# Kernel optimization log

Hardware: AMD Instinct MI355X
Metric: run time of the kernel (lower is better)

The kernel has to match this reference:

```python
import jax, jax.numpy as jnp
import numpy as np


def _gcn_norm(edge_index, num_nodes, dtype):
    # PyG GCNConv.norm: add self-loops (weight 1), symmetric deg^{-1/2} normalization
    row, col = edge_index[0], edge_index[1]
    loop = jnp.arange(num_nodes, dtype=row.dtype)
    row = jnp.concatenate([row, loop])
    col = jnp.concatenate([col, loop])
    ew = jnp.ones(row.shape[0], dtype=dtype)
    deg = jax.ops.segment_sum(ew, row, num_segments=num_nodes)
    dis = jnp.where(deg > 0, jax.lax.rsqrt(deg), 0.0)
    norm = dis[row] * ew * dis[col]
    return row, col, norm


def _masked_gcn_conv(x, row, col, norm, sigma, W, b, num_nodes):
    # mask_features: edge gather -> diff/sigma -> square -> scatter-add -> exp mask
    h = (x[col] - x[row]) / sigma            # [E, F]
    h = norm[:, None] * h * h                # [E, F]
    mask = jax.ops.segment_sum(h, row, num_segments=num_nodes)        # [N, F]
    deg = jax.ops.segment_sum(jnp.ones_like(norm), row, num_segments=num_nodes)  # degree(source), >=1 due to self-loops
    x = x * jnp.exp(-mask / deg[:, None])
    # GCNConv: linear transform then normalized aggregation source->target
    xw = x @ W                               # [N, O]
    out = jax.ops.segment_sum(norm[:, None] * xw[row], col, num_segments=num_nodes)
    return out + b


def setup_inputs() -> dict:
    key = jax.random.key(0)
    ks = jax.random.split(key, 8)
    N, E, F, H, C = 100000, 1600000, 128, 64, 40
    g = 1.414  # xavier gain used for sigma
    return {
        "x": jax.random.normal(ks[0], (N, F), jnp.float32),
        "edge_index": jax.random.randint(ks[1], (2, E), 0, N, jnp.int64),
        "sigma1": jax.random.uniform(ks[2], (1, F), jnp.float32, -1.0, 1.0) * (g * np.sqrt(6.0 / (1 + F))),
        "W1": jax.random.normal(ks[3], (F, H), jnp.float32) * (1.0 / np.sqrt(F)),
        "b1": jnp.zeros((H,), jnp.float32),
        "sigma2": jax.random.uniform(ks[4], (1, H), jnp.float32, -1.0, 1.0) * (g * np.sqrt(6.0 / (1 + H))),
        "W2": jax.random.normal(ks[5], (H, C), jnp.float32) * (1.0 / np.sqrt(H)),
        "b2": jnp.zeros((C,), jnp.float32),
    }


def reference(x, edge_index, sigma1, W1, b1, sigma2, W2, b2):
    N = x.shape[0]
    row, col, norm = _gcn_norm(edge_index, N, x.dtype)
    x = _masked_gcn_conv(x, row, col, norm, sigma1, W1, b1, N)
    x = jax.nn.relu(x)
    # dropout is identity in eval mode
    x = _masked_gcn_conv(x, row, col, norm, sigma2, W2, b2, N)
    return jax.nn.log_softmax(x, axis=1)
```

## Files before the change

### kernel.cpp

```cpp
#include <hip/hip_runtime.h>
#include <cmath>

constexpr int F1 = 128;
constexpr int H  = 64;
constexpr int NC = 40;
constexpr int NXCD = 8;

constexpr int SCAN_TPB = 256;
constexpr int SCAN_IPT = 8;
constexpr int SCAN_EPB = SCAN_TPB * SCAN_IPT;

__device__ inline unsigned short f2bf(float f) {
    union { float f; unsigned u; } v; v.f = f;
    return (unsigned short)((v.u + 0x7FFFu + ((v.u >> 16) & 1u)) >> 16);
}
__device__ inline float bflo(unsigned p) { union { float f; unsigned u; } v; v.u = p << 16; return v.f; }
__device__ inline float bfhi(unsigned p) { union { float f; unsigned u; } v; v.u = p & 0xFFFF0000u; return v.f; }
__device__ inline void unpack8(uint4 raw, float* d) {
    d[0] = bflo(raw.x); d[1] = bfhi(raw.x); d[2] = bflo(raw.y); d[3] = bfhi(raw.y);
    d[4] = bflo(raw.z); d[5] = bfhi(raw.z); d[6] = bflo(raw.w); d[7] = bfhi(raw.w);
}

__global__ void isg_kernel(const float* __restrict__ s1, float* __restrict__ i1,
                           const float* __restrict__ s2, float* __restrict__ i2) {
    int i = threadIdx.x;
    if (i < F1) i1[i] = 1.0f / s1[i];
    if (i < H)  i2[i] = 1.0f / s2[i];
}

__global__ void count8_prep_kernel(const int* __restrict__ row, const int* __restrict__ col,
                                   int* __restrict__ cntO, int* __restrict__ cntI,
                                   int E, int chunk, int stride, int cntBlocks,
                                   const float* __restrict__ x, const float* __restrict__ isg,
                                   unsigned short* __restrict__ u, size_t n8) {
    int bid = blockIdx.x;
    if (bid < cntBlocks) {
        int p = bid & (NXCD - 1);
        int gid = bid >> 3;
        unsigned lo = (unsigned)(p * chunk);
        for (int e = gid * blockDim.x + threadIdx.x; e < E; e += stride) {
            int r = row[e], c = col[e];
            if ((unsigned)r - lo < (unsigned)chunk) atomicAdd(&cntO[r], 1);
            if ((unsigned)c - lo < (unsigned)chunk) atomicAdd(&cntI[c], 1);
        }
    } else {
        size_t idx = (size_t)(bid - cntBlocks) * blockDim.x + threadIdx.x;
        if (idx >= n8) return;
        size_t base = idx * 8;
        int fk = (int)(base % (size_t)F1);
        float4 a0 = *(const float4*)&x[base];
        float4 a1 = *(const float4*)&x[base + 4];
        float4 s0 = *(const float4*)&isg[fk];
        float4 s1 = *(const float4*)&isg[fk + 4];
        uint4 p4;
        p4.x = (unsigned)f2bf(a0.x * s0.x) | ((unsigned)f2bf(a0.y * s0.y) << 16);
        p4.y = (unsigned)f2bf(a0.z * s0.z) | ((unsigned)f2bf(a0.w * s0.w) << 16);
        p4.z = (unsigned)f2bf(a1.x * s1.x) | ((unsigned)f2bf(a1.y * s1.y) << 16);
        p4.w = (unsigned)f2bf(a1.z * s1.z) | ((unsigned)f2bf(a1.w * s1.w) << 16);
        *(uint4*)&u[base] = p4;
    }
}

__global__ void scan_partial_kernel(const int* __restrict__ cnt, int* __restrict__ bsum, int M) {
    __shared__ int red[SCAN_TPB];
    int t = threadIdx.x;
    int i0 = blockIdx.x * SCAN_EPB + t * SCAN_IPT;
    int s = 0;
#pragma unroll
    for (int k = 0; k < SCAN_IPT; ++k) {
        int i = i0 + k;
        if (i < M) s += cnt[i];
    }
    red[t] = s;
    __syncthreads();
    for (int off = SCAN_TPB / 2; off > 0; off >>= 1) {
        if (t < off) red[t] += red[t + off];
        __syncthreads();
    }
    if (t == 0) bsum[blockIdx.x] = red[0];
}

__global__ void scan_offsets_kernel(int* __restrict__ bsum, int nb,
                                    int* __restrict__ rowptrO, int* __restrict__ rowptrI,
                                    int N, int E) {
    __shared__ int sh[1024];
    int t = threadIdx.x;
    sh[t] = (t < nb) ? bsum[t] : 0;
    __syncthreads();
    for (int off = 1; off < 1024; off <<= 1) {
        int v = (t >= off) ? sh[t - off] : 0;
        __syncthreads();
        sh[t] += v;
        __syncthreads();
    }
    if (t < nb) bsum[t] = (t > 0) ? sh[t - 1] : 0;
    if (t == 0) { rowptrO[N] = E; rowptrI[N] = E; }
}

__global__ void scan_final_kernel(int* __restrict__ cntO, int* __restrict__ cntI,
                                  const int* __restrict__ bsum,
                                  int* __restrict__ rowptrO, int* __restrict__ rowptrI,
                                  float* __restrict__ dis, int N, int E) {
    __shared__ int sh[SCAN_TPB];
    int t = threadIdx.x;
    int M = 2 * N;
    const int* cnt = cntO;
    int i0 = blockIdx.x * SCAN_EPB + t * SCAN_IPT;
    int cv[SCAN_IPT], pre[SCAN_IPT];
    int run = 0;
#pragma unroll
    for (int k = 0; k < SCAN_IPT; ++k) {
        int i = i0 + k;
        cv[k] = (i < M) ? cnt[i] : 0;
        pre[k] = run;
        run += cv[k];
    }
    sh[t] = run;
    __syncthreads();
    for (int off = 1; off < SCAN_TPB; off <<= 1) {
        int v = (t >= off) ? sh[t - off] : 0;
        __syncthreads();
        sh[t] += v;
        __syncthreads();
    }
    int toff = ((t > 0) ? sh[t - 1] : 0) + bsum[blockIdx.x];
#pragma unroll
    for (int k = 0; k < SCAN_IPT; ++k) {
        int i = i0 + k;
        if (i < M) {
            int val = toff + pre[k];
            if (i < N) {
                rowptrO[i] = val;
                cntO[i] = val;
                dis[i] = rsqrtf((float)(cv[k] + 1));
            } else {
                rowptrI[i - N] = val - E;
                cntI[i - N] = val - E;
            }
        }
    }
}

__global__ void build8_kernel(const int* __restrict__ row, const int* __restrict__ col,
                              int* __restrict__ curO, int* __restrict__ curI,
                              int2* __restrict__ adjO2, int2* __restrict__ adjI2,
                              const float* __restrict__ dis,
                              int E, int chunk, int stride) {
    int p = blockIdx.x & (NXCD - 1);
    int gid = blockIdx.x >> 3;
    unsigned lo = (unsigned)(p * chunk);
    for (int e = gid * blockDim.x + threadIdx.x; e < E; e += stride) {
        int r = row[e], c = col[e];
        bool inR = (unsigned)r - lo < (unsigned)chunk;
        bool inC = (unsigned)c - lo < (unsigned)chunk;
        if (inR | inC) {
            float nrm = dis[r] * dis[c];
            int nb = __float_as_int(nrm);
            if (inR) adjO2[atomicAdd(&curO[r], 1)] = make_int2(c, nb);
            if (inC) adjI2[atomicAdd(&curI[c], 1)] = make_int2(r, nb);
        }
    }
}

template<int F, int O, int R>
__global__ void fused_mask_gemm_kernel(const int* __restrict__ rowptr, const int2* __restrict__ adj2,
                                       const float* __restrict__ x,
                                       const unsigned short* __restrict__ u,
                                       const float* __restrict__ W,
                                       unsigned short* __restrict__ Ybf, int N) {
    constexpr int NT = R * 64;
    constexpr int G = F / 8;
    constexpr int NPI = 64 / G;
    __shared__ __align__(16) float Ws[F * O];
    __shared__ __align__(16) float Xs[R][F];
    int tid = threadIdx.x;
    for (int i = tid; i < F * O; i += NT) Ws[i] = W[i];
    int w = tid >> 6, lane = tid & 63;
    int h = lane / G, j = lane % G;
    int r = blockIdx.x * R + w;
    if (r < N) {
        int beg = rowptr[r], end = rowptr[r + 1];
        float inv_deg = 1.0f / (float)(end - beg + 1);
        float ur[8], acc[8];
        unpack8(*(const uint4*)&u[(size_t)r * F + 8 * j], ur);
#pragma unroll
        for (int k = 0; k < 8; ++k) acc[k] = 0.0f;
        for (int t = beg; t < end; t += 2 * NPI) {
            int e0 = t + h, e1 = t + NPI + h;
            int2 a0 = adj2[min(e0, end - 1)];
            int2 a1 = adj2[min(e1, end - 1)];
            float n0 = (e0 < end) ? __int_as_float(a0.y) : 0.0f;
            float n1 = (e1 < end) ? __int_as_float(a1.y) : 0.0f;
            uint4 rw0 = *(const uint4*)&u[(size_t)a0.x * F + 8 * j];
            uint4 rw1 = *(const uint4*)&u[(size_t)a1.x * F + 8 * j];
            float uc[8];
            unpack8(rw0, uc);
#pragma unroll
            for (int q = 0; q < 8; ++q) {
                float d = uc[q] - ur[q];
                acc[q] = fmaf(n0 * d, d, acc[q]);
            }
            unpack8(rw1, uc);
#pragma unroll
            for (int q = 0; q < 8; ++q) {
                float d = uc[q] - ur[q];
                acc[q] = fmaf(n1 * d, d, acc[q]);
            }
        }
#pragma unroll
        for (int off = G; off < 64; off <<= 1) {
#pragma unroll
            for (int k = 0; k < 8; ++k) acc[k] += __shfl_xor(acc[k], off);
        }
        if (h == 0) {
            float4 a0 = *(const float4*)&x[(size_t)r * F + 8 * j];
            float4 a1 = *(const float4*)&x[(size_t)r * F + 8 * j + 4];
            float xm[8] = {a0.x, a0.y, a0.z, a0.w, a1.x, a1.y, a1.z, a1.w};
#pragma unroll
            for (int k = 0; k < 8; ++k) xm[k] *= expf(-acc[k] * inv_deg);
            *(float4*)&Xs[w][8 * j]     = make_float4(xm[0], xm[1], xm[2], xm[3]);
            *(float4*)&Xs[w][8 * j + 4] = make_float4(xm[4], xm[5], xm[6], xm[7]);
        }
    }
    __syncthreads();
    if (r < N && lane < O) {
        float acc = 0.0f;
#pragma unroll
        for (int fq = 0; fq < F / 4; ++fq) {
            float4 xs = *(const float4*)&Xs[w][4 * fq];
            acc = fmaf(xs.x, Ws[(4 * fq + 0) * O + lane], acc);
            acc = fmaf(xs.y, Ws[(4 * fq + 1) * O + lane], acc);
            acc = fmaf(xs.z, Ws[(4 * fq + 2) * O + lane], acc);
            acc = fmaf(xs.w, Ws[(4 * fq + 3) * O + lane], acc);
        }
        float other = __shfl_xor(acc, 1);
        if (!(lane & 1)) {
            *(unsigned*)&Ybf[(size_t)r * O + lane] =
                (unsigned)f2bf(acc) | ((unsigned)f2bf(other) << 16);
        }
    }
}

__global__ void agg_relu_kernel(const int* __restrict__ rowptr, const int2* __restrict__ adj2,
                                const float* __restrict__ dis, const unsigned short* __restrict__ ybf,
                                const float* __restrict__ bias, float* __restrict__ h1,
                                unsigned short* __restrict__ u2, const float* __restrict__ isg2, int N) {
    int c = blockIdx.x * (blockDim.x >> 6) + (threadIdx.x >> 6);
    if (c >= N) return;
    int lane = threadIdx.x & 63;
    int h = lane >> 3, j = lane & 7;
    int beg = rowptr[c], end = rowptr[c + 1];
    float acc[8];
#pragma unroll
    for (int k = 0; k < 8; ++k) acc[k] = 0.0f;
    for (int t = beg; t < end; t += 16) {
        int e0 = t + h, e1 = t + 8 + h;
        int2 a0 = adj2[min(e0, end - 1)];
        int2 a1 = adj2[min(e1, end - 1)];
        float n0 = (e0 < end) ? __int_as_float(a0.y) : 0.0f;
        float n1 = (e1 < end) ? __int_as_float(a1.y) : 0.0f;
        uint4 rw0 = *(const uint4*)&ybf[(size_t)a0.x * H + 8 * j];
        uint4 rw1 = *(const uint4*)&ybf[(size_t)a1.x * H + 8 * j];
        float v[8];
        unpack8(rw0, v);
#pragma unroll
        for (int q = 0; q < 8; ++q) acc[q] = fmaf(n0, v[q], acc[q]);
        unpack8(rw1, v);
#pragma unroll
        for (int q = 0; q < 8; ++q) acc[q] = fmaf(n1, v[q], acc[q]);
    }
#pragma unroll
    for (int off = 8; off < 64; off <<= 1) {
#pragma unroll
        for (int k = 0; k < 8; ++k) acc[k] += __shfl_xor(acc[k], off);
    }
    if (h == 0) {
        float dc = dis[c];
        float sv[8];
        unpack8(*(const uint4*)&ybf[(size_t)c * H + 8 * j], sv);
        float4 b0 = *(const float4*)&bias[8 * j];
        float4 b1v = *(const float4*)&bias[8 * j + 4];
        float bb[8] = {b0.x, b0.y, b0.z, b0.w, b1v.x, b1v.y, b1v.z, b1v.w};
        float4 s0 = *(const float4*)&isg2[8 * j];
        float4 s1 = *(const float4*)&isg2[8 * j + 4];
        float sg[8] = {s0.x, s0.y, s0.z, s0.w, s1.x, s1.y, s1.z, s1.w};
        float hv[8];
        float d2 = dc * dc;
#pragma unroll
        for (int k = 0; k < 8; ++k) hv[k] = fmaxf(fmaf(d2, sv[k], acc[k]) + bb[k], 0.0f);
        *(float4*)&h1[(size_t)c * H + 8 * j]     = make_float4(hv[0], hv[1], hv[2], hv[3]);
        *(float4*)&h1[(size_t)c * H + 8 * j + 4] = make_float4(hv[4], hv[5], hv[6], hv[7]);
        uint4 p;
        p.x = (unsigned)f2bf(hv[0] * sg[0]) | ((unsigned)f2bf(hv[1] * sg[1]) << 16);
        p.y = (unsigned)f2bf(hv[2] * sg[2]) | ((unsigned)f2bf(hv[3] * sg[3]) << 16);
        p.z = (unsigned)f2bf(hv[4] * sg[4]) | ((unsigned)f2bf(hv[5] * sg[5]) << 16);
        p.w = (unsigned)f2bf(hv[6] * sg[6]) | ((unsigned)f2bf(hv[7] * sg[7]) << 16);
        *(uint4*)&u2[(size_t)c * H + 8 * j] = p;
    }
}

__global__ void agg_lsm_kernel(const int* __restrict__ rowptr, const int2* __restrict__ adj2,
                               const float* __restrict__ dis, const unsigned short* __restrict__ ybf,
                               const float* __restrict__ bias, float* __restrict__ out, int N) {
    int c = blockIdx.x * (blockDim.x >> 6) + (threadIdx.x >> 6);
    if (c >= N) return;
    int lane = threadIdx.x & 63;
    int h = lane >> 4, j = lane & 15;
    bool active = j < 10;
    int beg = rowptr[c], end = rowptr[c + 1];
    float a[4] = {0.f, 0.f, 0.f, 0.f};
    for (int t = beg; t < end; t += 8) {
        int e0 = t + h, e1 = t + 4 + h;
        int2 a0 = adj2[min(e0, end - 1)];
        int2 a1 = adj2[min(e1, end - 1)];
        float n0 = (e0 < end) ? __int_as_float(a0.y) : 0.0f;
        float n1 = (e1 < end) ? __int_as_float(a1.y) : 0.0f;
        uint2 rw0 = active ? *(const uint2*)&ybf[(size_t)a0.x * NC + 4 * j] : make_uint2(0u, 0u);
        uint2 rw1 = active ? *(const uint2*)&ybf[(size_t)a1.x * NC + 4 * j] : make_uint2(0u, 0u);
        a[0] = fmaf(n0, bflo(rw0.x), a[0]); a[1] = fmaf(n0, bfhi(rw0.x), a[1]);
        a[2] = fmaf(n0, bflo(rw0.y), a[2]); a[3] = fmaf(n0, bfhi(rw0.y), a[3]);
        a[0] = fmaf(n1, bflo(rw1.x), a[0]); a[1] = fmaf(n1, bfhi(rw1.x), a[1]);
        a[2] = fmaf(n1, bflo(rw1.y), a[2]); a[3] = fmaf(n1, bfhi(rw1.y), a[3]);
    }
#pragma unroll
    for (int off = 16; off < 64; off <<= 1) {
#pragma unroll
        for (int k = 0; k < 4; ++k) a[k] += __shfl_xor(a[k], off);
    }
    bool wr = (h == 0) && active;
    float v[4] = {-INFINITY, -INFINITY, -INFINITY, -INFINITY};
    if (wr) {
        float dc = dis[c];
        uint2 sr = *(const uint2*)&ybf[(size_t)c * NC + 4 * j];
        float sv[4] = {bflo(sr.x), bfhi(sr.x), bflo(sr.y), bfhi(sr.y)};
        float4 bb = *(const float4*)&bias[4 * j];
        float b4[4] = {bb.x, bb.y, bb.z, bb.w};
        float d2 = dc * dc;
#pragma unroll
        for (int k = 0; k < 4; ++k) v[k] = fmaf(d2, sv[k], a[k]) + b4[k];
    }
    float m = fmaxf(fmaxf(v[0], v[1]), fmaxf(v[2], v[3]));
#pragma unroll
    for (int off = 8; off > 0; off >>= 1) m = fmaxf(m, __shfl_xor(m, off));
    float s = wr ? (expf(v[0] - m) + expf(v[1] - m) + expf(v[2] - m) + expf(v[3] - m)) : 0.0f;
#pragma unroll
    for (int off = 8; off > 0; off >>= 1) s += __shfl_xor(s, off);
    float mls = m + logf(s);
    if (wr)
        *(float4*)&out[(size_t)c * NC + 4 * j] = make_float4(v[0] - mls, v[1] - mls, v[2] - mls, v[3] - mls);
}

extern "C" void kernel_launch(void* const* d_in, const int* in_sizes, int n_in,
                              void* d_out, int out_size, void* d_ws, size_t ws_size,
                              hipStream_t stream) {
    const float* x    = (const float*)d_in[0];
    const int*   ei   = (const int*)  d_in[1];
    const float* sig1 = (const float*)d_in[2];
    const float* W1   = (const float*)d_in[3];
    const float* b1   = (const float*)d_in[4];
    const float* sig2 = (const float*)d_in[5];
    const float* W2   = (const float*)d_in[6];
    const float* b2   = (const float*)d_in[7];
    float* out = (float*)d_out;

    const int N = in_sizes[0] / F1;
    const int E = in_sizes[1] / 2;
    const int* row = ei;
    const int* col = ei + E;

    char* w = (char*)d_ws;
    auto alloc = [&](size_t bytes) { void* q = w; w += (bytes + 255) & ~255ull; return q; };
    int*   cntO    = (int*)  alloc((size_t)2 * N * 4);
    int*   cntI    = cntO + N;
    int*   rowptrO = (int*)  alloc((size_t)(N + 1) * 4);
    int*   rowptrI = (int*)  alloc((size_t)(N + 1) * 4);
    int2*  adjO2   = (int2*) alloc((size_t)E * 8);
    int2*  adjI2   = (int2*) alloc((size_t)E * 8);
    float* dis     = (float*)alloc((size_t)N * 4);
    float* isg1    = (float*)alloc(F1 * 4);
    float* isg2    = (float*)alloc(H * 4);
    int*   bsum    = (int*)  alloc(1024 * 4);
    unsigned short* u1   = (unsigned short*)alloc((size_t)N * F1 * 2);
    unsigned short* u2   = (unsigned short*)alloc((size_t)N * H * 2);
    unsigned short* ybf1 = (unsigned short*)alloc((size_t)N * H * 2);
    float* h1      = (float*)alloc((size_t)N * H * 4);
    unsigned short* ybf2 = u1;

    const int B = 256;
    const int chunk = (N + NXCD - 1) / NXCD;
    const int WPP = 1024;
    const int stride8 = WPP * B;
    const int cntBlocks = NXCD * WPP;
    const size_t n8 = (size_t)N * F1 / 8;
    const int prepBlocks = (int)((n8 + B - 1) / B);
    const int M = 2 * N;
    const int nb = (M + SCAN_EPB - 1) / SCAN_EPB;

    hipMemsetAsync(cntO, 0, (size_t)2 * N * 4, stream);
    isg_kernel<<<1, 128, 0, stream>>>(sig1, isg1, sig2, isg2);
    count8_prep_kernel<<<cntBlocks + prepBlocks, B, 0, stream>>>(
        row, col, cntO, cntI, E, chunk, stride8, cntBlocks, x, isg1, u1, n8);
    scan_partial_kernel<<<nb, SCAN_TPB, 0, stream>>>(cntO, bsum, M);
    scan_offsets_kernel<<<1, 1024, 0, stream>>>(bsum, nb, rowptrO, rowptrI, N, E);
    scan_final_kernel<<<nb, SCAN_TPB, 0, stream>>>(cntO, cntI, bsum, rowptrO, rowptrI, dis, N, E);
    build8_kernel<<<cntBlocks, B, 0, stream>>>(row, col, cntO, cntI, adjO2, adjI2, dis, E, chunk, stride8);

    fused_mask_gemm_kernel<F1, H, 8><<<(N + 7) / 8, 512, 0, stream>>>(rowptrO, adjO2, x, u1, W1, ybf1, N);
    agg_relu_kernel<<<(N + 3) / 4, B, 0, stream>>>(rowptrI, adjI2, dis, ybf1, b1, h1, u2, isg2, N);

    fused_mask_gemm_kernel<H, NC, 8><<<(N + 7) / 8, 512, 0, stream>>>(rowptrO, adjO2, h1, u2, W2, ybf2, N);
    agg_lsm_kernel<<<(N + 3) / 4, B, 0, stream>>>(rowptrI, adjI2, dis, ybf2, b2, out, N);
}
```

Baseline: 632.7 us.

## Rebuild masked features from bf16 scaled copy and drop fp32 h1; use 4 partitions

The fused mask+GEMM kernel no longer reads the fp32 input row. It rebuilds x as u*sigma from the bf16 scaled copy it already holds in registers, which lets agg_relu skip writing the fp32 h1 buffer entirely. This removes a full fp32 N×F read per layer and an N×H fp32 write and buffer. The price is that the GEMM input now carries bf16 rounding. Separately, the count/build kernels switch from 8 node partitions to 4, each covering a larger chunk of nodes with more blocks per partition.

Result: faster. 614.0 us (-3.0%).

```diff
diff --git a/kernel.cpp b/kernel.cpp
--- a/kernel.cpp
+++ b/kernel.cpp
@@ -4,7 +4,7 @@
 constexpr int F1 = 128;
 constexpr int H  = 64;
 constexpr int NC = 40;
-constexpr int NXCD = 8;
+constexpr int NPART = 4;
 
 constexpr int SCAN_TPB = 256;
 constexpr int SCAN_IPT = 8;
@@ -35,8 +35,8 @@
                                    unsigned short* __restrict__ u, size_t n8) {
     int bid = blockIdx.x;
     if (bid < cntBlocks) {
-        int p = bid & (NXCD - 1);
-        int gid = bid >> 3;
+        int p = bid & (NPART - 1);
+        int gid = bid / NPART;
         unsigned lo = (unsigned)(p * chunk);
         for (int e = gid * blockDim.x + threadIdx.x; e < E; e += stride) {
             int r = row[e], c = col[e];
@@ -146,8 +146,8 @@
                               int2* __restrict__ adjO2, int2* __restrict__ adjI2,
                               const float* __restrict__ dis,
                               int E, int chunk, int stride) {
-    int p = blockIdx.x & (NXCD - 1);
-    int gid = blockIdx.x >> 3;
+    int p = blockIdx.x & (NPART - 1);
+    int gid = blockIdx.x / NPART;
     unsigned lo = (unsigned)(p * chunk);
     for (int e = gid * blockDim.x + threadIdx.x; e < E; e += stride) {
         int r = row[e], c = col[e];
@@ -164,7 +164,7 @@
 
 template<int F, int O, int R>
 __global__ void fused_mask_gemm_kernel(const int* __restrict__ rowptr, const int2* __restrict__ adj2,
-                                       const float* __restrict__ x,
+                                       const float* __restrict__ sig,
                                        const unsigned short* __restrict__ u,
                                        const float* __restrict__ W,
                                        unsigned short* __restrict__ Ybf, int N) {
@@ -213,11 +213,12 @@
             for (int k = 0; k < 8; ++k) acc[k] += __shfl_xor(acc[k], off);
         }
         if (h == 0) {
-            float4 a0 = *(const float4*)&x[(size_t)r * F + 8 * j];
-            float4 a1 = *(const float4*)&x[(size_t)r * F + 8 * j + 4];
-            float xm[8] = {a0.x, a0.y, a0.z, a0.w, a1.x, a1.y, a1.z, a1.w};
-#pragma unroll
-            for (int k = 0; k < 8; ++k) xm[k] *= expf(-acc[k] * inv_deg);
+            float4 s0 = *(const float4*)&sig[8 * j];
+            float4 s1 = *(const float4*)&sig[8 * j + 4];
+            float sg[8] = {s0.x, s0.y, s0.z, s0.w, s1.x, s1.y, s1.z, s1.w};
+            float xm[8];
+#pragma unroll
+            for (int k = 0; k < 8; ++k) xm[k] = ur[k] * sg[k] * expf(-acc[k] * inv_deg);
             *(float4*)&Xs[w][8 * j]     = make_float4(xm[0], xm[1], xm[2], xm[3]);
             *(float4*)&Xs[w][8 * j + 4] = make_float4(xm[4], xm[5], xm[6], xm[7]);
         }
@@ -243,7 +244,7 @@
 
 __global__ void agg_relu_kernel(const int* __restrict__ rowptr, const int2* __restrict__ adj2,
                                 const float* __restrict__ dis, const unsigned short* __restrict__ ybf,
-                                const float* __restrict__ bias, float* __restrict__ h1,
+                                const float* __restrict__ bias,
                                 unsigned short* __restrict__ u2, const float* __restrict__ isg2, int N) {
     int c = blockIdx.x * (blockDim.x >> 6) + (threadIdx.x >> 6);
     if (c >= N) return;
@@ -288,8 +289,6 @@
         float d2 = dc * dc;
 #pragma unroll
         for (int k = 0; k < 8; ++k) hv[k] = fmaxf(fmaf(d2, sv[k], acc[k]) + bb[k], 0.0f);
-        *(float4*)&h1[(size_t)c * H + 8 * j]     = make_float4(hv[0], hv[1], hv[2], hv[3]);
-        *(float4*)&h1[(size_t)c * H + 8 * j + 4] = make_float4(hv[4], hv[5], hv[6], hv[7]);
         uint4 p;
         p.x = (unsigned)f2bf(hv[0] * sg[0]) | ((unsigned)f2bf(hv[1] * sg[1]) << 16);
         p.y = (unsigned)f2bf(hv[2] * sg[2]) | ((unsigned)f2bf(hv[3] * sg[3]) << 16);
@@ -383,14 +382,12 @@
     unsigned short* u1   = (unsigned short*)alloc((size_t)N * F1 * 2);
     unsigned short* u2   = (unsigned short*)alloc((size_t)N * H * 2);
     unsigned short* ybf1 = (unsigned short*)alloc((size_t)N * H * 2);
-    float* h1      = (float*)alloc((size_t)N * H * 4);
     unsigned short* ybf2 = u1;
 
     const int B = 256;
-    const int chunk = (N + NXCD - 1) / NXCD;
-    const int WPP = 1024;
-    const int stride8 = WPP * B;
-    const int cntBlocks = NXCD * WPP;
+    const int chunk = (N + NPART - 1) / NPART;
+    const int TOTB = 8192;
+    const int stride4 = (TOTB / NPART) * B;
     const size_t n8 = (size_t)N * F1 / 8;
     const int prepBlocks = (int)((n8 + B - 1) / B);
     const int M = 2 * N;
@@ -398,16 +395,16 @@
 
     hipMemsetAsync(cntO, 0, (size_t)2 * N * 4, stream);
     isg_kernel<<<1, 128, 0, stream>>>(sig1, isg1, sig2, isg2);
-    count8_prep_kernel<<<cntBlocks + prepBlocks, B, 0, stream>>>(
-        row, col, cntO, cntI, E, chunk, stride8, cntBlocks, x, isg1, u1, n8);
+    count8_prep_kernel<<<TOTB + prepBlocks, B, 0, stream>>>(
+        row, col, cntO, cntI, E, chunk, stride4, TOTB, x, isg1, u1, n8);
     scan_partial_kernel<<<nb, SCAN_TPB, 0, stream>>>(cntO, bsum, M);
     scan_offsets_kernel<<<1, 1024, 0, stream>>>(bsum, nb, rowptrO, rowptrI, N, E);
     scan_final_kernel<<<nb, SCAN_TPB, 0, stream>>>(cntO, cntI, bsum, rowptrO, rowptrI, dis, N, E);
-    build8_kernel<<<cntBlocks, B, 0, stream>>>(row, col, cntO, cntI, adjO2, adjI2, dis, E, chunk, stride8);
-
-    fused_mask_gemm_kernel<F1, H, 8><<<(N + 7) / 8, 512, 0, stream>>>(rowptrO, adjO2, x, u1, W1, ybf1, N);
-    agg_relu_kernel<<<(N + 3) / 4, B, 0, stream>>>(rowptrI, adjI2, dis, ybf1, b1, h1, u2, isg2, N);
-
-    fused_mask_gemm_kernel<H, NC, 8><<<(N + 7) / 8, 512, 0, stream>>>(rowptrO, adjO2, h1, u2, W2, ybf2, N);
+    build8_kernel<<<TOTB, B, 0, stream>>>(row, col, cntO, cntI, adjO2, adjI2, dis, E, chunk, stride4);
+
+    fused_mask_gemm_kernel<F1, H, 8><<<(N + 7) / 8, 512, 0, stream>>>(rowptrO, adjO2, sig1, u1, W1, ybf1, N);
+    agg_relu_kernel<<<(N + 3) / 4, B, 0, stream>>>(rowptrI, adjI2, dis, ybf1, b1, u2, isg2, N);
+
+    fused_mask_gemm_kernel<H, NC, 8><<<(N + 7) / 8, 512, 0, stream>>>(rowptrO, adjO2, sig2, u2, W2, ybf2, N);
     agg_lsm_kernel<<<(N + 3) / 4, B, 0, stream>>>(rowptrI, adjI2, dis, ybf2, b2, out, N);
 }
```
